# Performance work log

Hardware: AMD Instinct MI355X
Metric: run time of the kernel (lower is better)

## Reference

```python
import jax, jax.numpy as jnp
import numpy as np

N_EMBD = 1024
N_HEAD = 16
HEAD_SIZE = 64
EPS = 1e-5


def _layer_norm(x, gamma, beta, eps=EPS):
    mu = jnp.mean(x, axis=-1, keepdims=True)
    var = jnp.mean(jnp.square(x - mu), axis=-1, keepdims=True)
    return (x - mu) * jax.lax.rsqrt(var + eps) * gamma + beta


def setup_inputs() -> dict:
    key = jax.random.key(0)
    ks = jax.random.split(key, 10)
    C = N_EMBD
    s = 1.0 / np.sqrt(C)
    x = jax.random.normal(ks[0], (4, 2048, C), dtype=jnp.float32)
    Wq = jax.random.normal(ks[1], (C, C), dtype=jnp.float32) * s
    Wk = jax.random.normal(ks[2], (C, C), dtype=jnp.float32) * s
    Wv = jax.random.normal(ks[3], (C, C), dtype=jnp.float32) * s
    Wo = jax.random.normal(ks[4], (C, C), dtype=jnp.float32) * s
    W1 = jax.random.normal(ks[5], (C, 4 * C), dtype=jnp.float32) * s
    b1 = jnp.zeros((4 * C,), dtype=jnp.float32)
    W2 = jax.random.normal(ks[6], (4 * C, C), dtype=jnp.float32) * (1.0 / np.sqrt(4 * C))
    b2 = jnp.zeros((C,), dtype=jnp.float32)
    g1 = jnp.ones((C,), dtype=jnp.float32)
    be1 = jnp.zeros((C,), dtype=jnp.float32)
    g2 = jnp.ones((C,), dtype=jnp.float32)
    be2 = jnp.zeros((C,), dtype=jnp.float32)
    return {"x": x, "Wq": Wq, "Wk": Wk, "Wv": Wv, "Wo": Wo,
            "W1": W1, "b1": b1, "W2": W2, "b2": b2,
            "g1": g1, "be1": be1, "g2": g2, "be2": be2}


def _block(x, Wq, Wk, Wv, Wo, W1, b1, W2, b2, g1, be1, g2, be2):
    B, T, C = x.shape
    H, D = N_HEAD, HEAD_SIZE
    # attention sub-block
    h = _layer_norm(x, g1, be1)
    q = (h @ Wq.T).reshape(B, T, H, D).transpose(0, 2, 1, 3)  # [B,H,T,D]
    k = (h @ Wk.T).reshape(B, T, H, D).transpose(0, 2, 1, 3)
    v = (h @ Wv.T).reshape(B, T, H, D).transpose(0, 2, 1, 3)
    wei = jnp.einsum("bhqd,bhkd->bhqk", q, k) * (D ** -0.5)
    causal = jnp.tril(jnp.ones((T, T), dtype=bool))
    wei = jnp.where(causal, wei, -jnp.inf)
    wei = jax.nn.softmax(wei, axis=-1)
    out = jnp.einsum("bhqk,bhkd->bhqd", wei, v)
    out = out.transpose(0, 2, 1, 3).reshape(B, T, C)
    x = x + out @ Wo.T
    # FFN sub-block (exact erf GELU, matching torch default)
    h2 = _layer_norm(x, g2, be2)
    ff = jax.nn.gelu(h2 @ W1 + b1, approximate=False) @ W2 + b2
    return x + ff


def reference(x, Wq, Wk, Wv, Wo, W1, b1, W2, b2, g1, be1, g2, be2):
    return _block(x, Wq, Wk, Wv, Wo, W1, b1, W2, b2, g1, be1, g2, be2)
```

## Files before the change

### kernel.cpp

```cpp
#include <hip/hip_runtime.h>
#include <cmath>

typedef unsigned short u16;
typedef __attribute__((ext_vector_type(8))) short bf16x8;
typedef __attribute__((ext_vector_type(4))) float f32x4;

#define TT 2048
#define CC 1024
#define BT 8192

__device__ __forceinline__ u16 f2bf(float f) {
  unsigned u = __builtin_bit_cast(unsigned, f);
  u += 0x7fffu + ((u >> 16) & 1u);
  return (u16)(u >> 16);
}

__device__ __forceinline__ float gelu_tanh(float v) {
  float u2 = v * (1.595769122f + 0.071354816f * v * v);
  return v / (1.f + __expf(-u2));
}

__device__ __forceinline__ void gload_lds16(const void* g, void* l) {
  __builtin_amdgcn_global_load_lds(
      (const __attribute__((address_space(1))) void*)g,
      (__attribute__((address_space(3))) void*)l, 16, 0, 0);
}


__global__ __launch_bounds__(256) void cvt_kernel(const float* __restrict__ s,
                                                  u16* __restrict__ d) {
  int i = (blockIdx.x * 256 + threadIdx.x) * 4;
  float4 v = *(const float4*)(s + i);
  ushort4 o;
  o.x = f2bf(v.x); o.y = f2bf(v.y); o.z = f2bf(v.z); o.w = f2bf(v.w);
  *(ushort4*)(d + i) = o;
}

__global__ __launch_bounds__(256) void transpose_cvt(const float* __restrict__ src,
                                                     u16* __restrict__ dst,
                                                     int R, int C) {
  __shared__ float tile[32][33];
  int c0 = blockIdx.x * 32, r0 = blockIdx.y * 32;
  int tx = threadIdx.x, ty = threadIdx.y;
#pragma unroll
  for (int j = 0; j < 4; ++j)
    tile[ty + j * 8][tx] = src[(size_t)(r0 + ty + j * 8) * C + c0 + tx];
  __syncthreads();
#pragma unroll
  for (int j = 0; j < 4; ++j)
    dst[(size_t)(c0 + ty + j * 8) * R + r0 + tx] = f2bf(tile[tx][ty + j * 8]);
}


__global__ __launch_bounds__(256) void ln_kernel(const float* __restrict__ x,
                                                 const float* __restrict__ gw,
                                                 const float* __restrict__ bw,
                                                 u16* __restrict__ out) {
  int row = blockIdx.x;
  int tid = threadIdx.x;
  const size_t base = (size_t)row * CC;
  float4 v = *(const float4*)(x + base + tid * 4);
  float s = v.x + v.y + v.z + v.w;
  float q = v.x * v.x + v.y * v.y + v.z * v.z + v.w * v.w;
#pragma unroll
  for (int o = 32; o > 0; o >>= 1) {
    s += __shfl_down(s, o, 64);
    q += __shfl_down(q, o, 64);
  }
  __shared__ float red[8];
  __shared__ float stat[2];
  int lane = tid & 63, wid = tid >> 6;
  if (!lane) { red[wid] = s; red[4 + wid] = q; }
  __syncthreads();
  if (!tid) {
    float S = red[0] + red[1] + red[2] + red[3];
    float Q = red[4] + red[5] + red[6] + red[7];
    float mu = S * (1.0f / CC);
    float var = Q * (1.0f / CC) - mu * mu;
    stat[0] = mu;
    stat[1] = rsqrtf(var + 1e-5f);
  }
  __syncthreads();
  float mu = stat[0], rs = stat[1];
  int c = tid * 4;
  float4 gv = *(const float4*)(gw + c);
  float4 bv = *(const float4*)(bw + c);
  ushort4 o;
  o.x = f2bf((v.x - mu) * rs * gv.x + bv.x);
  o.y = f2bf((v.y - mu) * rs * gv.y + bv.y);
  o.z = f2bf((v.z - mu) * rs * gv.z + bv.z);
  o.w = f2bf((v.w - mu) * rs * gv.w + bv.w);
  *(ushort4*)(out + base + c) = o;
}


template <int EPI>
__global__ __launch_bounds__(512) void gemm256(const u16* __restrict__ A,
                                               const u16* __restrict__ B,
                                               void* __restrict__ Cv,
                                               const float* __restrict__ bias,
                                               const float* __restrict__ resid,
                                               u16* __restrict__ vt,
                                               int N, int K, int gn) {
  __shared__ u16 lds[8][8192];
  const int tid = threadIdx.x, lane = tid & 63, wid = tid >> 6;
  const int nwg = gridDim.x;
  const int bid = blockIdx.x;
  const int sb = (nwg & 7) ? bid : ((bid & 7) * (nwg >> 3) + (bid >> 3));
  const int tM = (sb / gn) * 256, tN = (sb % gn) * 256;
  const int wm = wid >> 2, wn = wid & 3;
  const int fr = lane & 15, g4 = lane >> 4;
  const int gsw = (g4 ^ ((fr >> 3) << 1)) * 8;
  const int srow0 = wid * 16 + (lane >> 2);
  const int scol = ((lane & 3) ^ ((lane >> 5) << 1)) * 8;
  const u16* pA = A + (size_t)tM * K + (size_t)srow0 * K + scol;
  const u16* pB = B + (size_t)tN * K + (size_t)srow0 * K + scol;
  const int NKT = K >> 6;
  f32x4 acc[8][4] = {};

  auto stage = [&](int idx) {
    int kof = (idx >> 1) << 5;
    const u16* G = (idx & 1) ? pB : pA;
    u16* dst = &lds[idx & 7][wid * 512];
    gload_lds16(G + kof, dst);
    gload_lds16(G + (size_t)128 * K + kof, dst + 4096);
  };

#pragma unroll
  for (int j = 0; j < 4; ++j) stage(j);
  asm volatile("s_waitcnt vmcnt(4)" ::: "memory");
#pragma unroll
  for (int j = 4; j < 7; ++j) stage(j);
  asm volatile("s_waitcnt vmcnt(6)" ::: "memory");
  __builtin_amdgcn_s_barrier();

  for (int t2 = 0; t2 < NKT; t2 += 2) {
#pragma unroll
    for (int tt = 0; tt < 2; ++tt) {
      const int t = t2 + tt;
      const int bo = tt << 2;
#pragma unroll
      for (int ks = 0; ks < 2; ++ks) {
        const u16* Ah = lds[bo | (ks << 1)];
        const u16* Bh = lds[bo | (ks << 1) | 1];
        bf16x8 bfr[4];
#pragma unroll
        for (int ni = 0; ni < 4; ++ni)
          bfr[ni] = *(const bf16x8*)&Bh[(wn * 64 + ni * 16 + fr) * 32 + gsw];
#pragma unroll
        for (int mh = 0; mh < 2; ++mh) {
          bf16x8 af[4];
#pragma unroll
          for (int mi = 0; mi < 4; ++mi)
            af[mi] = *(const bf16x8*)&Ah[(wm * 128 + mh * 64 + mi * 16 + fr) * 32 + gsw];
          __builtin_amdgcn_sched_barrier(0);
          int idx = 4 * t + (ks << 1) + mh + 7;
          if (idx < 4 * NKT) stage(idx);
          __builtin_amdgcn_s_barrier();
          asm volatile("s_waitcnt lgkmcnt(0)" ::: "memory");
          __builtin_amdgcn_sched_barrier(0);
          __builtin_amdgcn_s_setprio(1);
#pragma unroll
          for (int mi = 0; mi < 4; ++mi)
#pragma unroll
            for (int ni = 0; ni < 4; ++ni)
              acc[mh * 4 + mi][ni] = __builtin_amdgcn_mfma_f32_16x16x32_bf16(
                  af[mi], bfr[ni], acc[mh * 4 + mi][ni], 0, 0, 0);
          __builtin_amdgcn_s_setprio(0);
          __builtin_amdgcn_sched_barrier(0);
          if (ks == 1 && mh == 1) {
            if (t < NKT - 2) asm volatile("s_waitcnt vmcnt(6)" ::: "memory");
            else if (t == NKT - 2) asm volatile("s_waitcnt vmcnt(0)" ::: "memory");
          }
          __builtin_amdgcn_s_barrier();
        }
      }
    }
  }

#pragma unroll
  for (int m = 0; m < 8; ++m) {
#pragma unroll
    for (int ni = 0; ni < 4; ++ni) {
      const int gR0 = tM + wm * 128 + m * 16 + g4 * 4;
      const int gC = tN + wn * 64 + ni * 16 + fr;
      if constexpr (EPI == 4) {
        if (gC < 2048) {
          float sc = (gC < 1024) ? 0.125f : 1.0f;
#pragma unroll
          for (int r = 0; r < 4; ++r)
            ((u16*)Cv)[(size_t)(gR0 + r) * 3072 + gC] = f2bf(acc[m][ni][r] * sc);
        } else {
          int tr = gR0 & 2047, bb = gR0 >> 11;
          int dv = gC - 2048, hh = dv >> 6, dd = dv & 63;
          int k5 = tr & 31;
          int pos = ((k5 & 15) >> 2) * 8 + ((k5 >> 4) & 1) * 4;
          ushort4 q4;
          q4.x = f2bf(acc[m][ni][0]);
          q4.y = f2bf(acc[m][ni][1]);
          q4.z = f2bf(acc[m][ni][2]);
          q4.w = f2bf(acc[m][ni][3]);
          *(ushort4*)&vt[((size_t)((bb * 16 + hh) * 64 + dd)) * 2048 + (tr & ~31) + pos] = q4;
        }
      } else if constexpr (EPI == 2) {
#pragma unroll
        for (int r = 0; r < 4; ++r) {
          float v = gelu_tanh(acc[m][ni][r] + bias[gC]);
          ((u16*)Cv)[(size_t)(gR0 + r) * N + gC] = f2bf(v);
        }
      } else {
#pragma unroll
        for (int r = 0; r < 4; ++r) {
          size_t idx = (size_t)(gR0 + r) * N + gC;
          float v = acc[m][ni][r] + resid[idx];
          if constexpr (EPI == 3) v += bias[gC];
          ((float*)Cv)[idx] = v;
        }
      }
    }
  }
}


__global__ __launch_bounds__(256) void attn_kernel(const u16* __restrict__ qkv,
                                                   const u16* __restrict__ vt,
                                                   u16* __restrict__ out) {
  const int pair = blockIdx.x;
  const int bh = blockIdx.y;
  const int b = bh >> 4, h = bh & 15;
  const int tid = threadIdx.x, lane = tid & 63, wid = tid >> 6;
  const int ql = lane & 15, g = lane >> 4;
  const int sw = ql & 7;
  __shared__ u16 Ks[2][4096];
  __shared__ u16 Vs[2][4096];
  const size_t rowQbase = (size_t)b * TT;
  const u16* kpart = qkv + rowQbase * 3072 + 1024 + h * 64;
  const u16* vpart = vt + ((size_t)(b * 16 + h) * 64) * 2048;
  const int srow = lane >> 3;
  const int sc16 = lane & 7;

  for (int pass = 0; pass < 2; ++pass) {
    const int qt = pass ? (31 - pair) : pair;
    const int qrow0 = qt * 64 + wid * 16;
    const int q_glb = qrow0 + ql;
    const u16* qp = qkv + (rowQbase + q_glb) * 3072 + h * 64 + g * 8;
    bf16x8 qf0 = *(const bf16x8*)qp;
    bf16x8 qf1 = *(const bf16x8*)(qp + 32);
    f32x4 o[4] = {};
    float m_run = -1e30f, l_run = 0.f;
    const int nt = qt + 1;

    auto stage = [&](int bufi, int t) {
      int kv0 = t * 64;
#pragma unroll
      for (int i = 0; i < 2; ++i) {
        int seg = wid * 2 + i;
        int rloc = seg * 8 + srow;
        int cs = (sc16 ^ (rloc & 7)) * 8;
        gload_lds16(kpart + (size_t)(kv0 + rloc) * 3072 + cs, &Ks[bufi][seg * 512]);
        gload_lds16(vpart + (size_t)rloc * 2048 + kv0 + cs, &Vs[bufi][seg * 512]);
      }
    };

    stage(0, 0);
    __syncthreads();
    int buf = 0;
    for (int t = 0; t < nt; ++t) {
      if (t + 1 < nt) stage(buf ^ 1, t + 1);
      const u16* Kb = Ks[buf];
      const u16* Vb = Vs[buf];
      const int kv0 = t * 64;
      float p[16];
#pragma unroll
      for (int kt = 0; kt < 4; ++kt) {
        int row = kt * 16 + ql;
        bf16x8 k0 = *(const bf16x8*)&Kb[row * 64 + ((g ^ sw) * 8)];
        bf16x8 k1 = *(const bf16x8*)&Kb[row * 64 + (((4 + g) ^ sw) * 8)];
        f32x4 s = {0.f, 0.f, 0.f, 0.f};
        s = __builtin_amdgcn_mfma_f32_16x16x32_bf16(k0, qf0, s, 0, 0, 0);
        s = __builtin_amdgcn_mfma_f32_16x16x32_bf16(k1, qf1, s, 0, 0, 0);
        if (t == qt) {
#pragma unroll
          for (int r = 0; r < 4; ++r) {
            int k_glb = kv0 + kt * 16 + 4 * g + r;
            p[kt * 4 + r] = (k_glb <= q_glb) ? s[r] : -1e30f;
          }
        } else {
#pragma unroll
          for (int r = 0; r < 4; ++r) p[kt * 4 + r] = s[r];
        }
      }
      float mloc = p[0];
#pragma unroll
      for (int i = 1; i < 16; ++i) mloc = fmaxf(mloc, p[i]);
      mloc = fmaxf(mloc, __shfl_xor(mloc, 16));
      mloc = fmaxf(mloc, __shfl_xor(mloc, 32));
      float mnew = fmaxf(m_run, mloc);
      float alpha = __expf(m_run - mnew);
      float lloc = 0.f;
      bf16x8 pa0, pa1;
#pragma unroll
      for (int i = 0; i < 16; ++i) {
        float e = __expf(p[i] - mnew);
        lloc += e;
        if (i < 8) pa0[i] = (short)f2bf(e);
        else pa1[i - 8] = (short)f2bf(e);
      }
      lloc += __shfl_xor(lloc, 16);
      lloc += __shfl_xor(lloc, 32);
      l_run = l_run * alpha + lloc;
      m_run = mnew;
      float aO[4];
#pragma unroll
      for (int r = 0; r < 4; ++r) aO[r] = __shfl(alpha, 4 * g + r);
#pragma unroll
      for (int d0 = 0; d0 < 4; ++d0) {
#pragma unroll
        for (int r = 0; r < 4; ++r) o[d0][r] *= aO[r];
      }
#pragma unroll
      for (int d0 = 0; d0 < 4; ++d0) {
        int row = d0 * 16 + ql;
        bf16x8 v0 = *(const bf16x8*)&Vb[row * 64 + ((g ^ sw) * 8)];
        bf16x8 v1 = *(const bf16x8*)&Vb[row * 64 + (((4 + g) ^ sw) * 8)];
        o[d0] = __builtin_amdgcn_mfma_f32_16x16x32_bf16(pa0, v0, o[d0], 0, 0, 0);
        o[d0] = __builtin_amdgcn_mfma_f32_16x16x32_bf16(pa1, v1, o[d0], 0, 0, 0);
      }
      __syncthreads();
      buf ^= 1;
    }
    float linv = 1.0f / l_run;
    float lO[4];
#pragma unroll
    for (int r = 0; r < 4; ++r) lO[r] = __shfl(linv, 4 * g + r);
#pragma unroll
    for (int d0 = 0; d0 < 4; ++d0) {
#pragma unroll
      for (int r = 0; r < 4; ++r) {
        size_t idx = (rowQbase + qrow0 + 4 * g + r) * CC + h * 64 + d0 * 16 + ql;
        out[idx] = f2bf(o[d0][r] * lO[r]);
      }
    }
  }
}


extern "C" void kernel_launch(void* const* d_in, const int* in_sizes, int n_in,
                              void* d_out, int out_size, void* d_ws, size_t ws_size,
                              hipStream_t stream) {
  const float* x   = (const float*)d_in[0];
  const float* Wq  = (const float*)d_in[1];
  const float* Wk  = (const float*)d_in[2];
  const float* Wv  = (const float*)d_in[3];
  const float* Wo  = (const float*)d_in[4];
  const float* W1  = (const float*)d_in[5];
  const float* b1  = (const float*)d_in[6];
  const float* W2  = (const float*)d_in[7];
  const float* b2  = (const float*)d_in[8];
  const float* g1  = (const float*)d_in[9];
  const float* be1 = (const float*)d_in[10];
  const float* g2  = (const float*)d_in[11];
  const float* be2 = (const float*)d_in[12];

  char* ws = (char*)d_ws;
  size_t off = 0;
  u16* Wqkv = (u16*)(ws + off); off += (size_t)3072 * 1024 * 2;
  u16* Wob  = (u16*)(ws + off); off += (size_t)1024 * 1024 * 2;
  u16* W1T  = (u16*)(ws + off); off += (size_t)4096 * 1024 * 2;
  u16* W2T  = (u16*)(ws + off); off += (size_t)1024 * 4096 * 2;
  u16* Hb   = (u16*)(ws + off); off += (size_t)BT * 1024 * 2;
  u16* QKV  = (u16*)(ws + off); off += (size_t)BT * 3072 * 2;
  u16* AttO = (u16*)(ws + off); off += (size_t)BT * 1024 * 2;
  float* X2 = (float*)(ws + off); off += (size_t)BT * 1024 * 4;
  u16* FF1 = QKV;
  u16* VT  = (u16*)X2;
  if (ws_size < off) return;

  cvt_kernel<<<1024, 256, 0, stream>>>(Wq, Wqkv);
  cvt_kernel<<<1024, 256, 0, stream>>>(Wk, Wqkv + 1024 * 1024);
  cvt_kernel<<<1024, 256, 0, stream>>>(Wv, Wqkv + 2 * 1024 * 1024);
  cvt_kernel<<<1024, 256, 0, stream>>>(Wo, Wob);
  transpose_cvt<<<dim3(128, 32), dim3(32, 8), 0, stream>>>(W1, W1T, 1024, 4096);
  transpose_cvt<<<dim3(32, 128), dim3(32, 8), 0, stream>>>(W2, W2T, 4096, 1024);

  ln_kernel<<<BT, 256, 0, stream>>>(x, g1, be1, Hb);
  gemm256<4><<<32 * 12, 512, 0, stream>>>(Hb, Wqkv, QKV, nullptr, nullptr, VT, 3072, 1024, 12);
  attn_kernel<<<dim3(16, 64), 256, 0, stream>>>(QKV, VT, AttO);
  gemm256<1><<<32 * 4, 512, 0, stream>>>(AttO, Wob, X2, nullptr, x, nullptr, 1024, 1024, 4);
  ln_kernel<<<BT, 256, 0, stream>>>(X2, g2, be2, Hb);
  gemm256<2><<<32 * 16, 512, 0, stream>>>(Hb, W1T, FF1, b1, nullptr, nullptr, 4096, 1024, 16);
  gemm256<3><<<32 * 4, 512, 0, stream>>>(FF1, W2T, (float*)d_out, b2, X2, nullptr, 1024, 4096, 4);
}
```

Measured before the change: 433.3 us.

## Split-K the FFN down-projection GEMM into two slices with reduction kernel

The final W2 GEMM (K=4096) now launches 256 workgroups split into two K halves instead of 128 full-K workgroups. Each half writes bf16 partial sums into the freed Hb and AttO buffers. A new elementwise kernel adds the two partials, the bias and the residual. The aim is better CU occupancy on a grid that was too small, at the cost of an extra kernel launch, extra memory traffic and bf16 rounding of the partial sums.

New measurement: 407.3 us. -6.0%, faster.

```diff
diff --git a/kernel.cpp b/kernel.cpp
--- a/kernel.cpp
+++ b/kernel.cpp
@@ -13,6 +13,10 @@
   unsigned u = __builtin_bit_cast(unsigned, f);
   u += 0x7fffu + ((u >> 16) & 1u);
   return (u16)(u >> 16);
+}
+
+__device__ __forceinline__ float bf2f(u16 u) {
+  return __builtin_bit_cast(float, (unsigned)u << 16);
 }
 
 __device__ __forceinline__ float gelu_tanh(float v) {
@@ -94,6 +98,26 @@
 }
 
 
+__global__ __launch_bounds__(256) void rf2_kernel(const u16* __restrict__ p0,
+                                                  const u16* __restrict__ p1,
+                                                  const float* __restrict__ b2,
+                                                  const float* __restrict__ resid,
+                                                  float* __restrict__ out) {
+  int c = threadIdx.x * 4;
+  size_t i = (size_t)blockIdx.x * CC + c;
+  ushort4 a = *(const ushort4*)(p0 + i);
+  ushort4 b = *(const ushort4*)(p1 + i);
+  float4 r = *(const float4*)(resid + i);
+  float4 bb = *(const float4*)(b2 + c);
+  float4 o;
+  o.x = bf2f(a.x) + bf2f(b.x) + r.x + bb.x;
+  o.y = bf2f(a.y) + bf2f(b.y) + r.y + bb.y;
+  o.z = bf2f(a.z) + bf2f(b.z) + r.z + bb.z;
+  o.w = bf2f(a.w) + bf2f(b.w) + r.w + bb.w;
+  *(float4*)(out + i) = o;
+}
+
+
 template <int EPI>
 __global__ __launch_bounds__(512) void gemm256(const u16* __restrict__ A,
                                                const u16* __restrict__ B,
@@ -101,20 +125,22 @@
                                                const float* __restrict__ bias,
                                                const float* __restrict__ resid,
                                                u16* __restrict__ vt,
-                                               int N, int K, int gn) {
+                                               int N, int K, int Kst,
+                                               int gn, int kdiv) {
   __shared__ u16 lds[8][8192];
   const int tid = threadIdx.x, lane = tid & 63, wid = tid >> 6;
   const int nwg = gridDim.x;
   const int bid = blockIdx.x;
   const int sb = (nwg & 7) ? bid : ((bid & 7) * (nwg >> 3) + (bid >> 3));
-  const int tM = (sb / gn) * 256, tN = (sb % gn) * 256;
+  const int kslice = sb / kdiv, rem = sb % kdiv;
+  const int tM = (rem / gn) * 256, tN = (rem % gn) * 256;
   const int wm = wid >> 2, wn = wid & 3;
   const int fr = lane & 15, g4 = lane >> 4;
   const int gsw = (g4 ^ ((fr >> 3) << 1)) * 8;
   const int srow0 = wid * 16 + (lane >> 2);
   const int scol = ((lane & 3) ^ ((lane >> 5) << 1)) * 8;
-  const u16* pA = A + (size_t)tM * K + (size_t)srow0 * K + scol;
-  const u16* pB = B + (size_t)tN * K + (size_t)srow0 * K + scol;
+  const u16* pA = A + (size_t)kslice * K + (size_t)tM * Kst + (size_t)srow0 * Kst + scol;
+  const u16* pB = B + (size_t)kslice * K + (size_t)tN * Kst + (size_t)srow0 * Kst + scol;
   const int NKT = K >> 6;
   f32x4 acc[8][4] = {};
 
@@ -123,7 +149,7 @@
     const u16* G = (idx & 1) ? pB : pA;
     u16* dst = &lds[idx & 7][wid * 512];
     gload_lds16(G + kof, dst);
-    gload_lds16(G + (size_t)128 * K + kof, dst + 4096);
+    gload_lds16(G + (size_t)128 * Kst + kof, dst + 4096);
   };
 
 #pragma unroll
@@ -202,6 +228,11 @@
           q4.w = f2bf(acc[m][ni][3]);
           *(ushort4*)&vt[((size_t)((bb * 16 + hh) * 64 + dd)) * 2048 + (tr & ~31) + pos] = q4;
         }
+      } else if constexpr (EPI == 0) {
+        u16* dst = kslice ? vt : (u16*)Cv;
+#pragma unroll
+        for (int r = 0; r < 4; ++r)
+          dst[(size_t)(gR0 + r) * N + gC] = f2bf(acc[m][ni][r]);
       } else if constexpr (EPI == 2) {
 #pragma unroll
         for (int r = 0; r < 4; ++r) {
@@ -375,6 +406,7 @@
   u16* FF1 = QKV;
   u16* VT  = (u16*)X2;
   if (ws_size < off) return;
+  const int KBIG = 1 << 20;
 
   cvt_kernel<<<1024, 256, 0, stream>>>(Wq, Wqkv);
   cvt_kernel<<<1024, 256, 0, stream>>>(Wk, Wqkv + 1024 * 1024);
@@ -384,10 +416,15 @@
   transpose_cvt<<<dim3(32, 128), dim3(32, 8), 0, stream>>>(W2, W2T, 4096, 1024);
 
   ln_kernel<<<BT, 256, 0, stream>>>(x, g1, be1, Hb);
-  gemm256<4><<<32 * 12, 512, 0, stream>>>(Hb, Wqkv, QKV, nullptr, nullptr, VT, 3072, 1024, 12);
+  gemm256<4><<<32 * 12, 512, 0, stream>>>(Hb, Wqkv, QKV, nullptr, nullptr, VT,
+                                          3072, 1024, 1024, 12, KBIG);
   attn_kernel<<<dim3(16, 64), 256, 0, stream>>>(QKV, VT, AttO);
-  gemm256<1><<<32 * 4, 512, 0, stream>>>(AttO, Wob, X2, nullptr, x, nullptr, 1024, 1024, 4);
+  gemm256<1><<<32 * 4, 512, 0, stream>>>(AttO, Wob, X2, nullptr, x, nullptr,
+                                         1024, 1024, 1024, 4, KBIG);
   ln_kernel<<<BT, 256, 0, stream>>>(X2, g2, be2, Hb);
-  gemm256<2><<<32 * 16, 512, 0, stream>>>(Hb, W1T, FF1, b1, nullptr, nullptr, 4096, 1024, 16);
-  gemm256<3><<<32 * 4, 512, 0, stream>>>(FF1, W2T, (float*)d_out, b2, X2, nullptr, 1024, 4096, 4);
-}
+  gemm256<2><<<32 * 16, 512, 0, stream>>>(Hb, W1T, FF1, b1, nullptr, nullptr,
+                                          4096, 1024, 1024, 16, KBIG);
+  gemm256<0><<<32 * 8, 512, 0, stream>>>(FF1, W2T, Hb, nullptr, nullptr, AttO,
+                                         1024, 2048, 4096, 4, 128);
+  rf2_kernel<<<BT, 256, 0, stream>>>(Hb, AttO, b2, X2, (float*)d_out);
+}
```
